# Optimization experiments

Hardware: AMD Instinct MI355X
Metric: run time of the kernel (lower is better)

## Reference

```python
import jax, jax.numpy as jnp
from jax import lax
import numpy as np


def setup_inputs() -> dict:
    key = jax.random.key(0)
    k1, k2, k3 = jax.random.split(key, 3)
    B, C_in, C_out, H, W_sp = 32, 256, 256, 56, 56
    x = jax.random.normal(k1, (B, C_in, H, W_sp), dtype=jnp.float32)
    # Full per-(out,in) 3x3 kernels; a structural mask (applied in reference)
    # zeros out the off-center taps of the 1x1 positions, matching HetConv.
    fan_in = 9.0  # each torch Conv2d(1,1,k) inits with its own fan-in; scale is
    # irrelevant for correctness testing, use a small uniform-ish init.
    W = jax.random.normal(k2, (C_out, C_in, 3, 3), dtype=jnp.float32) * (1.0 / np.sqrt(fan_in))
    b = jax.random.normal(k3, (C_out, C_in), dtype=jnp.float32) * 0.05
    return {"x": x, "W": W, "b": b, "p": 4}


def _het_mask(out_f, in_f, p):
    # mask[n, i] is full 3x3 when (i - n) % p == 0, else only the center tap
    n = jnp.arange(out_f)[:, None]
    i = jnp.arange(in_f)[None, :]
    is3x3 = ((i - n) % p == 0)  # [out, in]
    center = jnp.zeros((3, 3), jnp.float32).at[1, 1].set(1.0)
    full = jnp.ones((3, 3), jnp.float32)
    return jnp.where(is3x3[:, :, None, None], full, center)  # [out, in, 3, 3]


def reference(x, W, b, p):
    out_f, in_f = W.shape[0], W.shape[1]
    Wm = W * _het_mask(out_f, in_f, p)
    # Sum over input channels of per-channel convs == one dense NCHW conv.
    y = lax.conv_general_dilated(
        x, Wm, window_strides=(1, 1), padding=((1, 1), (1, 1)),
        dimension_numbers=("NCHW", "OIHW", "NCHW"))
    # Each (n, i) conv adds its own bias; total per output channel = sum_i b[n, i].
    return y + jnp.sum(b, axis=1)[None, :, None, None]
```

## Files before the change

### kernel.cpp

```cpp
#include <hip/hip_runtime.h>
#include <hip/hip_bf16.h>

#define BATCH 32
#define CIN   256
#define COUT  256
#define Hd    56
#define Wd    56
#define HW    (Hd*Wd)

typedef __attribute__((ext_vector_type(8))) short bf16x8;
typedef __attribute__((ext_vector_type(4))) short bf16x4;
typedef __attribute__((ext_vector_type(4))) float f32x4;

__device__ __forceinline__ unsigned short f2bf_rne(float f) {
    unsigned u = __builtin_bit_cast(unsigned, f);
    u += 0x7fffu + ((u >> 16) & 1u);
    return (unsigned short)(u >> 16);
}

__global__ __launch_bounds__(512) void hetconv_wprep(const float* __restrict__ W,
                                                     const float* __restrict__ bb_,
                                                     unsigned short* __restrict__ Wc3,
                                                     unsigned short* __restrict__ Wg3,
                                                     float* __restrict__ bsum) {
    const int bid = blockIdx.x;
    const int tid = threadIdx.x;
    const int lane = tid & 63;
    const int wid  = tid >> 6;

    if (bid < 48) {
        const int u = bid * 8 + wid;
        const int l15 = lane & 15;
        const int l4  = lane >> 4;
        if (u < 128) {
            const int mf = u & 3;
            const int ks = (u >> 2) & 1;
            const int p  = (u >> 3) & 3;
            const int r  = u >> 5;
            const int np = r * 64 + mf * 16 + l15;
            const int n  = ((np & 63) << 2) | r;
            #pragma unroll
            for (int e = 0; e < 8; ++e) {
                int kq = ks * 32 + l4 * 8 + e;
                int rr = kq >> 4, jj = kq & 15;
                int ic = (p * 16 + jj) * 4 + rr;
                Wc3[u * 512 + lane * 8 + e] = f2bf_rne(W[(n * CIN + ic) * 9 + 4]);
            }
        } else {
            const int u2 = u - 128;
            const int mf = u2 & 3;
            const int tp = (u2 >> 2) & 3;
            const int p  = (u2 >> 4) & 3;
            const int r  = u2 >> 6;
            const int np = r * 64 + mf * 16 + l15;
            const int n  = ((np & 63) << 2) | r;
            const int t8  = tp * 2 + (l4 >> 1);
            const int tap = t8 + (t8 >= 4);
            #pragma unroll
            for (int e = 0; e < 8; ++e) {
                int jj = (l4 & 1) * 8 + e;
                int ic = (p * 16 + jj) * 4 + r;
                Wg3[u2 * 512 + lane * 8 + e] = f2bf_rne(W[(n * CIN + ic) * 9 + tap]);
            }
        }
    } else {
        const int np = (bid - 48) * 8 + wid;
        const int n = ((np & 63) << 2) | (np >> 6);
        float s = 0.f;
        for (int i = lane; i < CIN; i += 64) s += bb_[n * CIN + i];
        #pragma unroll
        for (int off = 32; off > 0; off >>= 1) s += __shfl_down(s, off, 64);
        if (lane == 0) bsum[np] = s;
    }
}

__global__ __launch_bounds__(1024, 2) void hetconv_main(const float* __restrict__ x,
                             const unsigned short* __restrict__ Wc3,
                             const unsigned short* __restrict__ Wg3,
                             const float* __restrict__ bsum,
                             float* __restrict__ y) {
    __shared__ unsigned short xs[4][16384];

    const int bid  = blockIdx.x;
    const int work = (bid & 7) * 112 + (bid >> 3);
    const int b    = work / 28;
    const int R0   = (work % 28) * 2;
    const int tid = threadIdx.x;
    const int lane = tid & 63;
    const int wid  = tid >> 6;
    const int h  = wid & 1;
    const int mh = (wid >> 1) & 1;
    const int r  = wid >> 2;
    const int l15 = lane & 15;
    const int l4  = lane >> 4;

    const float* xbase = x + (size_t)b * CIN * HW;

    f32x4 acc[2][4];
    #pragma unroll
    for (int i = 0; i < 2; ++i)
        #pragma unroll
        for (int j = 0; j < 4; ++j) acc[i][j] = f32x4{0.f, 0.f, 0.f, 0.f};

    auto CONVERT = [&](int pass, unsigned short* dst) {
        const int a   = tid & 511;
        const int q   = a & 15;
        const int oct = ((a >> 4) & 3) | (((a >> 6) & 1) << 2);
        const int row = (a >> 7) & 3;
        const int grow = R0 - 1 + row;
        const bool ok = (grow >= 0) && (grow < Hd) && (q < 14);
        const float* xrow = xbase + (size_t)grow * Wd + q * 4;
        #pragma unroll 1
        for (int hf = 0; hf < 2; ++hf) {
            f32x4 v[4];
            #pragma unroll
            for (int e4 = 0; e4 < 4; ++e4) {
                int kq = oct * 8 + hf * 4 + e4;
                int rr = kq >> 4, jj = kq & 15;
                int ic = (pass * 16 + jj) * 4 + rr;
                v[e4] = ok ? *reinterpret_cast<const f32x4*>(xrow + (size_t)ic * HW)
                           : f32x4{0.f, 0.f, 0.f, 0.f};
            }
            #pragma unroll
            for (int i = 0; i < 4; ++i) {
                int col = q * 4 + i;
                bf16x4 pk;
                #pragma unroll
                for (int e4 = 0; e4 < 4; ++e4) pk[e4] = (short)f2bf_rne(v[e4][i]);
                *reinterpret_cast<bf16x4*>(
                    reinterpret_cast<char*>(dst) + (row * 64 + col) * 128
                    + ((oct ^ (col & 7)) << 4) + hf * 8) = pk;
            }
        }
    };

    auto COMPUTE = [&](int p) {
        const unsigned short* buf = xs[p];
        const int srow = (h + 1) * 64;
        #pragma unroll
        for (int ks = 0; ks < 2; ++ks) {
            bf16x8 a[2];
            #pragma unroll
            for (int mfl = 0; mfl < 2; ++mfl) {
                int chunk = r * 32 + p * 8 + ks * 4 + mh * 2 + mfl;
                a[mfl] = *reinterpret_cast<const bf16x8*>(
                    Wc3 + ((size_t)chunk << 9) + lane * 8);
            }
            #pragma unroll
            for (int nf = 0; nf < 4; ++nf) {
                int col = nf * 16 + l15;
                int pix = srow + col;
                int oct = ks * 4 + l4;
                int addr = pix * 128 + ((oct ^ (col & 7)) << 4);
                bf16x8 bbv = *reinterpret_cast<const bf16x8*>(
                    reinterpret_cast<const char*>(buf) + addr);
                #pragma unroll
                for (int mfl = 0; mfl < 2; ++mfl)
                    acc[mfl][nf] = __builtin_amdgcn_mfma_f32_16x16x32_bf16(
                        a[mfl], bbv, acc[mfl][nf], 0, 0, 0);
            }
        }
        #pragma unroll
        for (int tp = 0; tp < 4; ++tp) {
            const int t8  = tp * 2 + (l4 >> 1);
            const int tap = t8 + (t8 >= 4);
            const int dy  = tap / 3 - 1;
            const int dx  = tap % 3 - 1;
            const int lr  = h + 1 + dy;
            const int oct = r * 2 + (l4 & 1);
            bf16x8 ag[2];
            #pragma unroll
            for (int mfl = 0; mfl < 2; ++mfl) {
                int chunk = r * 64 + p * 16 + tp * 4 + mh * 2 + mfl;
                ag[mfl] = *reinterpret_cast<const bf16x8*>(
                    Wg3 + ((size_t)chunk << 9) + lane * 8);
            }
            #pragma unroll
            for (int nf = 0; nf < 4; ++nf) {
                int c2 = nf * 16 + l15 + dx;
                c2 = ((unsigned)c2 < 64u) ? c2 : 56;
                int pix  = lr * 64 + c2;
                int addr = pix * 128 + ((oct ^ (c2 & 7)) << 4);
                bf16x8 bbv = *reinterpret_cast<const bf16x8*>(
                    reinterpret_cast<const char*>(buf) + addr);
                #pragma unroll
                for (int mfl = 0; mfl < 2; ++mfl)
                    acc[mfl][nf] = __builtin_amdgcn_mfma_f32_16x16x32_bf16(
                        ag[mfl], bbv, acc[mfl][nf], 0, 0, 0);
            }
        }
    };

    const int hb = tid >> 9;
    CONVERT(hb, xs[hb]);
    __syncthreads();
    COMPUTE(0);
    CONVERT(2 + hb, xs[2 + hb]);
    COMPUTE(1);
    __syncthreads();
    COMPUTE(2);
    COMPUTE(3);
    __syncthreads();

    float* lf = reinterpret_cast<float*>(xs[0]);
    #pragma unroll
    for (int q = 0; q < 2; ++q) {
        if ((r >> 1) == q) {
            #pragma unroll
            for (int mfl = 0; mfl < 2; ++mfl) {
                #pragma unroll
                for (int j = 0; j < 4; ++j) {
                    int chL = (r & 1) * 64 + mh * 32 + mfl * 16 + l4 * 4 + j;
                    float bias = bsum[q * 128 + chL];
                    #pragma unroll
                    for (int nf = 0; nf < 4; ++nf) {
                        int col = nf * 16 + l15;
                        if (col < Wd)
                            lf[chL * 116 + h * 56 + col] = acc[mfl][nf][j] + bias;
                    }
                }
            }
        }
        __syncthreads();
        #pragma unroll
        for (int it = 0; it < 4; ++it) {
            int v = it * 1024 + tid;
            if (v < 3584) {
                int chL = v / 28;
                int f   = v % 28;
                int h2  = (f >= 14) ? 1 : 0;
                int colS = (f - h2 * 14) * 4;
                int n = ((chL & 63) << 2) | (q * 2 + (chL >> 6));
                f32x4 val = *reinterpret_cast<const f32x4*>(lf + chL * 116 + f * 4);
                __builtin_nontemporal_store(val, reinterpret_cast<f32x4*>(
                    y + (((size_t)b * COUT + n) * Hd + (R0 + h2)) * Wd + colS));
            }
        }
        __syncthreads();
    }
}

extern "C" void kernel_launch(void* const* d_in, const int* in_sizes, int n_in,
                              void* d_out, int out_size, void* d_ws, size_t ws_size,
                              hipStream_t stream) {
    const float* x = (const float*)d_in[0];
    const float* W = (const float*)d_in[1];
    const float* b = (const float*)d_in[2];
    float* y = (float*)d_out;

    unsigned short* Wc3  = (unsigned short*)d_ws;
    unsigned short* Wg3  = (unsigned short*)((char*)d_ws + 131072);
    float*          bsum = (float*)((char*)d_ws + 393216);

    hipLaunchKernelGGL(hetconv_wprep, dim3(80), dim3(512), 0, stream,
                       W, b, Wc3, Wg3, bsum);
    hipLaunchKernelGGL(hetconv_main, dim3(BATCH * 28), dim3(1024), 0, stream,
                       x, Wc3, Wg3, bsum, y);
}
```

Before: 87.58 us.

## Split input conversion across all threads and pipeline per-pass with compute

Each CONVERT call now has all 1024 threads handle one pass, each thread doing one half (hf) instead of looping over both halves while half the block serves each of two passes. The schedule becomes a per-pass software pipeline: pass p+1 is converted while pass p is computed, with a barrier after each stage. The goal is finer-grained overlap of global loads and bf16 conversion with MFMA work and a shorter prologue before compute starts. The cost is more __syncthreads barriers, five instead of three.

```diff
diff --git a/kernel.cpp b/kernel.cpp
--- a/kernel.cpp
+++ b/kernel.cpp
@@ -102,35 +102,33 @@
         #pragma unroll
         for (int j = 0; j < 4; ++j) acc[i][j] = f32x4{0.f, 0.f, 0.f, 0.f};
 
+    const int cq   = tid & 15;
+    const int coct = ((tid >> 4) & 3) | (((tid >> 6) & 1) << 2);
+    const int crow = (tid >> 7) & 3;
+    const int chf  = tid >> 9;
+    const int cgrow = R0 - 1 + crow;
+    const bool cok = (cgrow >= 0) && (cgrow < Hd) && (cq < 14);
+    const float* cxrow = xbase + (size_t)cgrow * Wd + cq * 4;
+
     auto CONVERT = [&](int pass, unsigned short* dst) {
-        const int a   = tid & 511;
-        const int q   = a & 15;
-        const int oct = ((a >> 4) & 3) | (((a >> 6) & 1) << 2);
-        const int row = (a >> 7) & 3;
-        const int grow = R0 - 1 + row;
-        const bool ok = (grow >= 0) && (grow < Hd) && (q < 14);
-        const float* xrow = xbase + (size_t)grow * Wd + q * 4;
-        #pragma unroll 1
-        for (int hf = 0; hf < 2; ++hf) {
-            f32x4 v[4];
-            #pragma unroll
-            for (int e4 = 0; e4 < 4; ++e4) {
-                int kq = oct * 8 + hf * 4 + e4;
-                int rr = kq >> 4, jj = kq & 15;
-                int ic = (pass * 16 + jj) * 4 + rr;
-                v[e4] = ok ? *reinterpret_cast<const f32x4*>(xrow + (size_t)ic * HW)
-                           : f32x4{0.f, 0.f, 0.f, 0.f};
-            }
-            #pragma unroll
-            for (int i = 0; i < 4; ++i) {
-                int col = q * 4 + i;
-                bf16x4 pk;
-                #pragma unroll
-                for (int e4 = 0; e4 < 4; ++e4) pk[e4] = (short)f2bf_rne(v[e4][i]);
-                *reinterpret_cast<bf16x4*>(
-                    reinterpret_cast<char*>(dst) + (row * 64 + col) * 128
-                    + ((oct ^ (col & 7)) << 4) + hf * 8) = pk;
-            }
+        f32x4 v[4];
+        #pragma unroll
+        for (int e4 = 0; e4 < 4; ++e4) {
+            int kq = coct * 8 + chf * 4 + e4;
+            int rr = kq >> 4, jj = kq & 15;
+            int ic = (pass * 16 + jj) * 4 + rr;
+            v[e4] = cok ? *reinterpret_cast<const f32x4*>(cxrow + (size_t)ic * HW)
+                        : f32x4{0.f, 0.f, 0.f, 0.f};
+        }
+        #pragma unroll
+        for (int i = 0; i < 4; ++i) {
+            int col = cq * 4 + i;
+            bf16x4 pk;
+            #pragma unroll
+            for (int e4 = 0; e4 < 4; ++e4) pk[e4] = (short)f2bf_rne(v[e4][i]);
+            *reinterpret_cast<bf16x4*>(
+                reinterpret_cast<char*>(dst) + (crow * 64 + col) * 128
+                + ((coct ^ (col & 7)) << 4) + chf * 8) = pk;
         }
     };
 
@@ -191,14 +189,14 @@
         }
     };
 
-    const int hb = tid >> 9;
-    CONVERT(hb, xs[hb]);
-    __syncthreads();
-    COMPUTE(0);
-    CONVERT(2 + hb, xs[2 + hb]);
-    COMPUTE(1);
-    __syncthreads();
-    COMPUTE(2);
+    CONVERT(0, xs[0]);
+    __syncthreads();
+    CONVERT(1, xs[1]);  COMPUTE(0);
+    __syncthreads();
+    CONVERT(2, xs[2]);  COMPUTE(1);
+    __syncthreads();
+    CONVERT(3, xs[3]);  COMPUTE(2);
+    __syncthreads();
     COMPUTE(3);
     __syncthreads();
 
```

Measured after the change: 94.87 us. 1.08x slower.
